# Kernel optimization log

Measured on AMD Instinct MI355X. Metric: run time of the kernel, lower is better.

## Reference

```python
import jax, jax.numpy as jnp
import numpy as np
from jax import lax

N_HEADS = 8
HEAD_DIM = 64
STATE = N_HEADS * HEAD_DIM  # 512
EPS = 1e-6


def setup_inputs() -> dict:
    key = jax.random.key(0)
    ks = jax.random.split(key, 6)
    B, S, D = 4, 4096, 1024
    x = jax.random.normal(ks[0], (B, S, D), jnp.float32)
    w_in = jax.random.normal(ks[1], (4 * STATE, D), jnp.float32) * 0.02
    conv_w = jax.random.normal(ks[2], (STATE, 1, 4), jnp.float32) * 0.5
    state_weight = jax.random.normal(ks[3], (3 * N_HEADS, HEAD_DIM, HEAD_DIM), jnp.float32) * 0.02
    norm_w = jnp.ones((STATE,), jnp.float32)
    w_out = jax.random.normal(ks[5], (D, STATE), jnp.float32) * 0.02
    return {"x": x, "w_in": w_in, "conv_w": conv_w, "state_weight": state_weight, "norm_w": norm_w, "w_out": w_out}


def _forward(x, w_in, conv_w, state_weight, norm_w, w_out):
    B, S, _ = x.shape
    proj = jnp.einsum('bsd,od->bso', x, w_in)  # [B,S,4*STATE]
    xi, xf, xr, g = jnp.split(proj, [STATE, 2 * STATE, 3 * STATE], axis=-1)

    # causal depthwise conv1d on xi (pad left k-1, groups = STATE), then silu
    K = conv_w.shape[-1]
    xi_c = xi.transpose(0, 2, 1)  # [B,C,S]
    xi_c = lax.conv_general_dilated(xi_c, conv_w, window_strides=(1,),
                                    padding=[(K - 1, 0)], feature_group_count=STATE)
    xi = jax.nn.silu(xi_c.transpose(0, 2, 1))  # [B,S,STATE]

    xi = xi.reshape(B, S, N_HEADS, HEAD_DIM)
    xf = xf.reshape(B, S, N_HEADS, HEAD_DIM)
    xr = xr.reshape(B, S, N_HEADS, HEAD_DIM)

    W = state_weight[:N_HEADS]
    Wf = state_weight[N_HEADS:2 * N_HEADS]
    Wr = state_weight[2 * N_HEADS:]

    def step(h, inp):
        xt, xft, xrt = inp  # each [B,N,H]
        f = jax.nn.sigmoid(jnp.einsum('bnh,nhk->bnk', h, Wf) + xft)
        r = jax.nn.sigmoid(jnp.einsum('bnh,nhk->bnk', h, Wr) + xrt)
        z = jnp.tanh(jnp.einsum('bnh,nhk->bnk', h * r, W) + xt)
        h_new = f * h + (1.0 - f) * z
        return h_new, h_new

    h0 = jnp.zeros((B, N_HEADS, HEAD_DIM), x.dtype)
    xs = (xi.transpose(1, 0, 2, 3), xf.transpose(1, 0, 2, 3), xr.transpose(1, 0, 2, 3))
    _, ys = lax.scan(step, h0, xs)  # [S,B,N,H]

    y = ys.transpose(1, 0, 2, 3).reshape(B, S, STATE)
    y = y * jax.nn.silu(g)
    # RMSNorm
    y = y * lax.rsqrt(jnp.mean(y * y, axis=-1, keepdims=True) + EPS) * norm_w
    return jnp.einsum('bss_,os_->bso'.replace('s_', 'c'), y, w_out)


def reference(x, w_in, conv_w, state_weight, norm_w, w_out):
    return _forward(x, w_in, conv_w, state_weight, norm_w, w_out)
```

## Files before the change

### kernel.cpp

```cpp
#include <hip/hip_runtime.h>
#include <hip/hip_bf16.h>
#include <cstddef>

#define B_      4
#define S_      4096
#define D_      1024
#define NH_     8
#define HD_     64
#define STATE_  512
#define PROJ_   2048
#define ROWS_   16384

typedef float f32x4 __attribute__((ext_vector_type(4)));
typedef __bf16 bf16x8 __attribute__((ext_vector_type(8)));
typedef _Float16 f16x2 __attribute__((ext_vector_type(2)));

__device__ __forceinline__ unsigned short bfbits(float f) {
    __hip_bfloat16 h = __float2bfloat16(f);
    return __builtin_bit_cast(unsigned short, h);
}

__device__ __forceinline__ float b2f(unsigned short u) {
    union { unsigned int i; float f; } v;
    v.i = ((unsigned int)u) << 16;
    return v.f;
}

__device__ __forceinline__ float fast_sigmoid(float x) {
    return __builtin_amdgcn_rcpf(1.0f + __expf(-x));
}

__device__ __forceinline__ float fast_tanh(float x) {
    return 1.0f - 2.0f * __builtin_amdgcn_rcpf(__expf(2.0f * x) + 1.0f);
}

__device__ __forceinline__ void async_copy16(void* lds, const void* g) {
    __builtin_amdgcn_global_load_lds(
        (const __attribute__((address_space(1))) unsigned int*)g,
        (__attribute__((address_space(3))) unsigned int*)lds,
        16, 0, 0);
}

__device__ __forceinline__ unsigned int pkf16(float a, float b) {
    auto h = __builtin_amdgcn_cvt_pkrtz(a, b);
    return __builtin_bit_cast(unsigned int, h);
}

__device__ __forceinline__ f16x2 u2h(unsigned int u) {
    return __builtin_bit_cast(f16x2, u);
}

__device__ __forceinline__ unsigned int rl_u32(unsigned int v, int lane) {
    return (unsigned int)__builtin_amdgcn_readlane((int)v, lane);
}

__device__ __forceinline__ float fdot2f(f16x2 a, f16x2 b, float c) {
    return __builtin_amdgcn_fdot2(a, b, c, false);
}

__device__ __forceinline__ unsigned int pack_pair(float v, bool oddlane) {
    int vb = __builtin_bit_cast(int, v);
    int pb = __builtin_amdgcn_mov_dpp(vb, 0xB1, 0xF, 0xF, true);
    float p = __builtin_bit_cast(float, pb);
    float lo = oddlane ? p : v;
    float hi = oddlane ? v : p;
    return pkf16(lo, hi);
}

__global__ __launch_bounds__(256) void f2bf(const float* __restrict__ in,
                                            unsigned short* __restrict__ out, int n4) {
    int i = blockIdx.x * 256 + threadIdx.x;
    if (i < n4) {
        float4 v = ((const float4*)in)[i];
        ushort4 o;
        o.x = bfbits(v.x); o.y = bfbits(v.y); o.z = bfbits(v.z); o.w = bfbits(v.w);
        ((ushort4*)out)[i] = o;
    }
}

__device__ __forceinline__ void store_out(float* p, float v) { *p = v; }
__device__ __forceinline__ void store_out(__hip_bfloat16* p, float v) { *p = __float2bfloat16(v); }

template <typename OutT>
__global__ __launch_bounds__(256, 1) void gemm_bt(const unsigned short* __restrict__ A,
                                                  const unsigned short* __restrict__ Bm,
                                                  OutT* __restrict__ C,
                                                  int M, int N, int K) {
    __shared__ __align__(16) unsigned short As[128 * 32];
    __shared__ __align__(16) unsigned short Bs[128 * 32];
    const int tid  = threadIdx.x;
    const int lane = tid & 63;
    const int w    = tid >> 6;
    const int wm   = w >> 1;
    const int wn   = w & 1;
    const int l16  = lane & 15;
    const int quad = lane >> 4;
    const int m0 = blockIdx.y * 128;
    const int n0 = blockIdx.x * 128;

    f32x4 acc[4][4] = {};

    const int off0 = w * 1024 + lane * 16;
    const int off1 = (w + 4) * 1024 + lane * 16;
    const int r0 = off0 >> 6, cb0 = off0 & 63;
    const int r1 = off1 >> 6, cb1 = off1 & 63;
    char* lA0 = (char*)As + w * 1024;
    char* lA1 = (char*)As + (w + 4) * 1024;
    char* lB0 = (char*)Bs + w * 1024;
    char* lB1 = (char*)Bs + (w + 4) * 1024;
    const size_t Kb = (size_t)K * 2;

    for (int k0 = 0; k0 < K; k0 += 32) {
        const char* a0 = (const char*)A + (size_t)(m0 + r0) * Kb + (size_t)k0 * 2 + cb0;
        const char* a1 = (const char*)A + (size_t)(m0 + r1) * Kb + (size_t)k0 * 2 + cb1;
        const char* b0 = (const char*)Bm + (size_t)(n0 + r0) * Kb + (size_t)k0 * 2 + cb0;
        const char* b1 = (const char*)Bm + (size_t)(n0 + r1) * Kb + (size_t)k0 * 2 + cb1;
        async_copy16(lA0, a0);
        async_copy16(lA1, a1);
        async_copy16(lB0, b0);
        async_copy16(lB1, b1);
        __syncthreads();

        bf16x8 af[4], bf[4];
#pragma unroll
        for (int mt = 0; mt < 4; ++mt) {
            int r = wm * 64 + mt * 16 + l16;
            af[mt] = *(const bf16x8*)(&As[r * 32 + quad * 8]);
        }
#pragma unroll
        for (int nt = 0; nt < 4; ++nt) {
            int r = wn * 64 + nt * 16 + l16;
            bf[nt] = *(const bf16x8*)(&Bs[r * 32 + quad * 8]);
        }
#pragma unroll
        for (int mt = 0; mt < 4; ++mt)
#pragma unroll
            for (int nt = 0; nt < 4; ++nt)
                acc[mt][nt] = __builtin_amdgcn_mfma_f32_16x16x32_bf16(af[mt], bf[nt], acc[mt][nt], 0, 0, 0);
        __syncthreads();
    }

#pragma unroll
    for (int mt = 0; mt < 4; ++mt) {
#pragma unroll
        for (int nt = 0; nt < 4; ++nt) {
            const int col = n0 + wn * 64 + nt * 16 + l16;
            const int row = m0 + wm * 64 + mt * 16 + quad * 4;
#pragma unroll
            for (int rg = 0; rg < 4; ++rg)
                store_out(&C[(size_t)(row + rg) * N + col], acc[mt][nt][rg]);
        }
    }
}

__global__ __launch_bounds__(256) void transpose_scan(const unsigned short* __restrict__ proj,
                                                      ushort4* __restrict__ sc) {
    const int idx = blockIdx.x * 256 + threadIdx.x;
    const int c   = idx & 511;
    const int row = idx >> 9;
    const int b = row >> 12, t = row & 4095;
    const int n = c >> 6, kk = c & 63;
    const unsigned short* src = proj + (size_t)row * PROJ_ + c;
    ushort4 v;
    v.x = src[0];
    v.y = src[512];
    v.z = src[1024];
    v.w = src[1536];
    sc[((size_t)(b * 8 + n) * S_ + t) * 64 + kk] = v;
}

#define SCAN_STEP(T, V)                                                        \
    {                                                                          \
        const float xi_raw = b2f(V.x);                                         \
        const float xf_v   = b2f(V.y);                                         \
        const float xr_v   = b2f(V.z);                                         \
        const float g_v    = b2f(V.w);                                         \
        {                       \
            const int tn = ((T) + 2 < S_) ? (T) + 2 : S_ - 1;                  \
            V = pin[(size_t)tn * 64];                                          \
        }                                                                      \
        float xc = fmaf(cw3, xi_raw, fmaf(cw2, xm1, fmaf(cw1, xm2, cw0 * xm3)));\
        xm3 = xm2; xm2 = xm1; xm1 = xi_raw;                                    \
        const float xi_v = xc * fast_sigmoid(xc);                              \
        const float gs_v = g_v * fast_sigmoid(g_v);                            \
        unsigned int hs[32];                                                   \
        _Pragma("unroll")                                                      \
        for (int p = 0; p < 32; ++p) hs[p] = rl_u32(hpk, 2 * p);               \
        __builtin_amdgcn_sched_barrier(0);                                     \
        float fa[4] = {xf_v, 0.f, 0.f, 0.f};                                   \
        float ra[4] = {xr_v, 0.f, 0.f, 0.f};                                   \
        _Pragma("unroll")                                                      \
        for (int p = 0; p < 32; ++p) {                                         \
            fa[p & 3] = fdot2f(u2h(hs[p]), u2h(Wf2[p]), fa[p & 3]);            \
            ra[p & 3] = fdot2f(u2h(hs[p]), u2h(Wr2[p]), ra[p & 3]);            \
        }                                                                      \
        const float f_v = fast_sigmoid((fa[0] + fa[1]) + (fa[2] + fa[3]));     \
        const float r_v = fast_sigmoid((ra[0] + ra[1]) + (ra[2] + ra[3]));     \
        const unsigned int hrpk = pack_pair(h_me * r_v, oddlane);              \
        __builtin_amdgcn_sched_barrier(0);                                     \
        unsigned int zs[32];                                                   \
        _Pragma("unroll")                                                      \
        for (int p = 0; p < 32; ++p) zs[p] = rl_u32(hrpk, 2 * p);              \
        __builtin_amdgcn_sched_barrier(0);                                     \
        float za[4] = {xi_v, 0.f, 0.f, 0.f};                                   \
        _Pragma("unroll")                                                      \
        for (int p = 0; p < 32; ++p)                                           \
            za[p & 3] = fdot2f(u2h(zs[p]), u2h(Wz2[p]), za[p & 3]);            \
        const float z_v = fast_tanh((za[0] + za[1]) + (za[2] + za[3]));        \
        const float hn  = fmaf(f_v, h_me - z_v, z_v);                          \
        h_me = hn;                                                             \
        hpk  = pack_pair(hn, oddlane);                                         \
        yout[(size_t)(T) * STATE_] = hn * gs_v;                                \
    }

__global__ __launch_bounds__(64)
__attribute__((amdgpu_waves_per_eu(1, 1)))
void scan_kernel(
    const ushort4* __restrict__ scanin,
    const float* __restrict__ conv_w,
    const float* __restrict__ sw,
    float* __restrict__ y)
{
    const int bn = blockIdx.x;
    const int b  = bn >> 3;
    const int n  = bn & 7;
    const int k  = threadIdx.x;
    const int c  = n * HD_ + k;
    const bool oddlane = (k & 1) != 0;

    unsigned int Wz2[32], Wf2[32], Wr2[32];
    {
        const float* wz = sw + (size_t)n * 4096 + k;
        const float* wf = wz + 8 * 4096;
        const float* wr = wz + 16 * 4096;
#pragma unroll
        for (int jp = 0; jp < 32; ++jp) {
            Wz2[jp] = pkf16(wz[(2 * jp) * 64], wz[(2 * jp + 1) * 64]);
            Wf2[jp] = pkf16(wf[(2 * jp) * 64], wf[(2 * jp + 1) * 64]);
            Wr2[jp] = pkf16(wr[(2 * jp) * 64], wr[(2 * jp + 1) * 64]);
        }
    }
    const float cw0 = conv_w[c * 4 + 0];
    const float cw1 = conv_w[c * 4 + 1];
    const float cw2 = conv_w[c * 4 + 2];
    const float cw3 = conv_w[c * 4 + 3];

    float h_me = 0.0f;
    unsigned int hpk = 0;
    float xm1 = 0.f, xm2 = 0.f, xm3 = 0.f;

    const ushort4* pin = scanin + (size_t)bn * S_ * 64 + k;
    float* yout = y + (size_t)b * S_ * STATE_ + c;

    ushort4 aV = pin[0];
    ushort4 bV = pin[64];

    for (int t = 0; t < S_; t += 2) {
        SCAN_STEP(t,     aV);
        SCAN_STEP(t + 1, bV);
    }
}

__global__ __launch_bounds__(128) void rmsnorm_bf16(const float* __restrict__ y,
                                                    const float* __restrict__ nw,
                                                    unsigned short* __restrict__ out) {
    const int row = blockIdx.x;
    const int t   = threadIdx.x;
    const float4 v = ((const float4*)(y + (size_t)row * STATE_))[t];
    float ss = fmaf(v.x, v.x, fmaf(v.y, v.y, fmaf(v.z, v.z, v.w * v.w)));
#pragma unroll
    for (int off = 32; off > 0; off >>= 1) ss += __shfl_xor(ss, off, 64);
    __shared__ float wred[2];
    if ((t & 63) == 0) wred[t >> 6] = ss;
    __syncthreads();
    const float tot   = wred[0] + wred[1];
    const float scale = rsqrtf(tot * (1.0f / (float)STATE_) + 1e-6f);
    const float4 w4 = ((const float4*)nw)[t];
    ushort4 o;
    o.x = bfbits(v.x * scale * w4.x);
    o.y = bfbits(v.y * scale * w4.y);
    o.z = bfbits(v.z * scale * w4.z);
    o.w = bfbits(v.w * scale * w4.w);
    ((ushort4*)out)[(size_t)row * (STATE_ / 4) + t] = o;
}

extern "C" void kernel_launch(void* const* d_in, const int* in_sizes, int n_in,
                              void* d_out, int out_size, void* d_ws, size_t ws_size,
                              hipStream_t stream) {
    const float* x      = (const float*)d_in[0];
    const float* w_in   = (const float*)d_in[1];
    const float* conv_w = (const float*)d_in[2];
    const float* sw     = (const float*)d_in[3];
    const float* norm_w = (const float*)d_in[4];
    const float* w_out  = (const float*)d_in[5];
    float* out = (float*)d_out;

    char* ws = (char*)d_ws;
    unsigned short* xbf     = (unsigned short*)(ws + 0);
    unsigned short* w_inbf  = (unsigned short*)(ws + 33554432);
    unsigned short* w_outbf = (unsigned short*)(ws + 37748736);
    ushort4*        scanin  = (ushort4*)(ws + 38797312);
    float*          yf      = (float*)(ws + 0);
    unsigned short* ybf     = (unsigned short*)(ws + 38797312);
    unsigned short* projbf  = (unsigned short*)d_out;

    f2bf<<<(ROWS_ * D_ / 4 + 255) / 256, 256, 0, stream>>>(x, xbf, ROWS_ * D_ / 4);
    f2bf<<<(PROJ_ * D_ / 4 + 255) / 256, 256, 0, stream>>>(w_in, w_inbf, PROJ_ * D_ / 4);
    f2bf<<<(D_ * STATE_ / 4 + 255) / 256, 256, 0, stream>>>(w_out, w_outbf, D_ * STATE_ / 4);

    gemm_bt<__hip_bfloat16><<<dim3(PROJ_ / 128, ROWS_ / 128), 256, 0, stream>>>(
        xbf, w_inbf, (__hip_bfloat16*)projbf, ROWS_, PROJ_, D_);

    transpose_scan<<<ROWS_ * 512 / 256, 256, 0, stream>>>(projbf, scanin);

    scan_kernel<<<32, 64, 0, stream>>>(scanin, conv_w, sw, yf);

    rmsnorm_bf16<<<ROWS_, 128, 0, stream>>>(yf, norm_w, ybf);

    gemm_bt<float><<<dim3(D_ / 128, ROWS_ / 128), 256, 0, stream>>>(
        ybf, w_outbf, out, ROWS_, D_, STATE_);
}
```

Measured before the change: 2.105 ms.

## Interleave four batch recurrences per wavefront in scan kernel for ILP

The scan kernel now runs one wavefront per head that advances all four batch sequences together, instead of one wavefront per (batch, head). The readlane broadcasts and dot products of independent batches are interleaved so that the serial latency of each recurrence step is hidden by work from the other batches. In exchange the grid shrinks from 32 to 8 wavefronts, so less of the GPU is used, and register pressure rises, with a possible risk of spills.

```diff
diff --git a/kernel.cpp b/kernel.cpp
--- a/kernel.cpp
+++ b/kernel.cpp
@@ -169,48 +169,76 @@
     sc[((size_t)(b * 8 + n) * S_ + t) * 64 + kk] = v;
 }
 
-#define SCAN_STEP(T, V)                                                        \
+
+#define SB __builtin_amdgcn_sched_barrier(0);
+
+#define DECODE(b, T, V)                                                        \
+    const float xf_##b = b2f(V.y);                                             \
+    const float xr_##b = b2f(V.z);                                             \
+    const float g_##b  = b2f(V.w);                                             \
+    float xc_##b;                                                              \
     {                                                                          \
         const float xi_raw = b2f(V.x);                                         \
-        const float xf_v   = b2f(V.y);                                         \
-        const float xr_v   = b2f(V.z);                                         \
-        const float g_v    = b2f(V.w);                                         \
-        {                       \
-            const int tn = ((T) + 2 < S_) ? (T) + 2 : S_ - 1;                  \
-            V = pin[(size_t)tn * 64];                                          \
-        }                                                                      \
-        float xc = fmaf(cw3, xi_raw, fmaf(cw2, xm1, fmaf(cw1, xm2, cw0 * xm3)));\
-        xm3 = xm2; xm2 = xm1; xm1 = xi_raw;                                    \
-        const float xi_v = xc * fast_sigmoid(xc);                              \
-        const float gs_v = g_v * fast_sigmoid(g_v);                            \
-        unsigned int hs[32];                                                   \
-        _Pragma("unroll")                                                      \
-        for (int p = 0; p < 32; ++p) hs[p] = rl_u32(hpk, 2 * p);               \
-        __builtin_amdgcn_sched_barrier(0);                                     \
-        float fa[4] = {xf_v, 0.f, 0.f, 0.f};                                   \
-        float ra[4] = {xr_v, 0.f, 0.f, 0.f};                                   \
-        _Pragma("unroll")                                                      \
-        for (int p = 0; p < 32; ++p) {                                         \
-            fa[p & 3] = fdot2f(u2h(hs[p]), u2h(Wf2[p]), fa[p & 3]);            \
-            ra[p & 3] = fdot2f(u2h(hs[p]), u2h(Wr2[p]), ra[p & 3]);            \
-        }                                                                      \
-        const float f_v = fast_sigmoid((fa[0] + fa[1]) + (fa[2] + fa[3]));     \
-        const float r_v = fast_sigmoid((ra[0] + ra[1]) + (ra[2] + ra[3]));     \
-        const unsigned int hrpk = pack_pair(h_me * r_v, oddlane);              \
-        __builtin_amdgcn_sched_barrier(0);                                     \
-        unsigned int zs[32];                                                   \
-        _Pragma("unroll")                                                      \
-        for (int p = 0; p < 32; ++p) zs[p] = rl_u32(hrpk, 2 * p);              \
-        __builtin_amdgcn_sched_barrier(0);                                     \
-        float za[4] = {xi_v, 0.f, 0.f, 0.f};                                   \
-        _Pragma("unroll")                                                      \
-        for (int p = 0; p < 32; ++p)                                           \
-            za[p & 3] = fdot2f(u2h(zs[p]), u2h(Wz2[p]), za[p & 3]);            \
-        const float z_v = fast_tanh((za[0] + za[1]) + (za[2] + za[3]));        \
-        const float hn  = fmaf(f_v, h_me - z_v, z_v);                          \
-        h_me = hn;                                                             \
-        hpk  = pack_pair(hn, oddlane);                                         \
-        yout[(size_t)(T) * STATE_] = hn * gs_v;                                \
+        const int tn = ((T) + 2 < S_) ? (T) + 2 : S_ - 1;                      \
+        V = pin_##b[(size_t)tn * 64];                                          \
+        xc_##b = fmaf(cw3, xi_raw,                                             \
+                 fmaf(cw2, xm1_##b, fmaf(cw1, xm2_##b, cw0 * xm3_##b)));       \
+        xm3_##b = xm2_##b; xm2_##b = xm1_##b; xm1_##b = xi_raw;                \
+    }                                                                          \
+    const float xiv_##b = xc_##b * fast_sigmoid(xc_##b);                       \
+    const float gsv_##b = g_##b * fast_sigmoid(g_##b);
+
+#define RLB(arr, src)                                                          \
+    _Pragma("unroll")                                                          \
+    for (int p = 0; p < 32; ++p) arr[p] = rl_u32(src, 2 * p);
+
+#define FRD(b, arr)                                                            \
+    float fa_##b[4] = {xf_##b, 0.f, 0.f, 0.f};                                 \
+    float ra_##b[4] = {xr_##b, 0.f, 0.f, 0.f};                                 \
+    _Pragma("unroll")                                                          \
+    for (int p = 0; p < 32; ++p) {                                             \
+        fa_##b[p & 3] = fdot2f(u2h(arr[p]), u2h(Wf2[p]), fa_##b[p & 3]);       \
+        ra_##b[p & 3] = fdot2f(u2h(arr[p]), u2h(Wr2[p]), ra_##b[p & 3]);       \
+    }
+
+#define GAT(b)                                                                 \
+    const float fv_##b = fast_sigmoid((fa_##b[0] + fa_##b[1]) +                \
+                                      (fa_##b[2] + fa_##b[3]));                \
+    const float rv_##b = fast_sigmoid((ra_##b[0] + ra_##b[1]) +                \
+                                      (ra_##b[2] + ra_##b[3]));                \
+    const unsigned int hr_##b = pack_pair(h_##b * rv_##b, oddlane);
+
+#define ZD(b, arr)                                                             \
+    float za_##b[4] = {xiv_##b, 0.f, 0.f, 0.f};                                \
+    _Pragma("unroll")                                                          \
+    for (int p = 0; p < 32; ++p)                                               \
+        za_##b[p & 3] = fdot2f(u2h(arr[p]), u2h(Wz2[p]), za_##b[p & 3]);
+
+#define UPD(b, T)                                                              \
+    {                                                                          \
+        const float zv = fast_tanh((za_##b[0] + za_##b[1]) +                   \
+                                   (za_##b[2] + za_##b[3]));                   \
+        const float hn = fmaf(fv_##b, h_##b - zv, zv);                         \
+        h_##b  = hn;                                                           \
+        hp_##b = pack_pair(hn, oddlane);                                       \
+        yout_##b[(size_t)(T) * STATE_] = hn * gsv_##b;                         \
+    }
+
+#define STEP4(T, V0, V1, V2, V3)                                               \
+    {                                                                          \
+        DECODE(0, T, V0) DECODE(1, T, V1) DECODE(2, T, V2) DECODE(3, T, V3)    \
+        unsigned int hsA[32], hsB[32];                                         \
+        RLB(hsA, hp_0) RLB(hsB, hp_1) SB                                       \
+        FRD(0, hsA) FRD(1, hsB) SB                                             \
+        RLB(hsA, hp_2) RLB(hsB, hp_3) SB                                       \
+        GAT(0) GAT(1)                                                          \
+        FRD(2, hsA) FRD(3, hsB) SB                                             \
+        GAT(2) GAT(3)                                                          \
+        RLB(hsA, hr_0) RLB(hsB, hr_1) SB                                       \
+        ZD(0, hsA) ZD(1, hsB) SB                                               \
+        RLB(hsA, hr_2) RLB(hsB, hr_3) SB                                       \
+        ZD(2, hsA) ZD(3, hsB)                                                  \
+        UPD(0, T) UPD(1, T) UPD(2, T) UPD(3, T)                                \
     }
 
 __global__ __launch_bounds__(64)
@@ -221,11 +249,9 @@
     const float* __restrict__ sw,
     float* __restrict__ y)
 {
-    const int bn = blockIdx.x;
-    const int b  = bn >> 3;
-    const int n  = bn & 7;
-    const int k  = threadIdx.x;
-    const int c  = n * HD_ + k;
+    const int n = blockIdx.x;
+    const int k = threadIdx.x;
+    const int c = n * HD_ + k;
     const bool oddlane = (k & 1) != 0;
 
     unsigned int Wz2[32], Wf2[32], Wr2[32];
@@ -245,19 +271,30 @@
     const float cw2 = conv_w[c * 4 + 2];
     const float cw3 = conv_w[c * 4 + 3];
 
-    float h_me = 0.0f;
-    unsigned int hpk = 0;
-    float xm1 = 0.f, xm2 = 0.f, xm3 = 0.f;
-
-    const ushort4* pin = scanin + (size_t)bn * S_ * 64 + k;
-    float* yout = y + (size_t)b * S_ * STATE_ + c;
-
-    ushort4 aV = pin[0];
-    ushort4 bV = pin[64];
+    float h_0 = 0.f, h_1 = 0.f, h_2 = 0.f, h_3 = 0.f;
+    unsigned int hp_0 = 0, hp_1 = 0, hp_2 = 0, hp_3 = 0;
+    float xm1_0 = 0.f, xm2_0 = 0.f, xm3_0 = 0.f;
+    float xm1_1 = 0.f, xm2_1 = 0.f, xm3_1 = 0.f;
+    float xm1_2 = 0.f, xm2_2 = 0.f, xm3_2 = 0.f;
+    float xm1_3 = 0.f, xm2_3 = 0.f, xm3_3 = 0.f;
+
+    const ushort4* pin_0 = scanin + (size_t)(0 * 8 + n) * S_ * 64 + k;
+    const ushort4* pin_1 = scanin + (size_t)(1 * 8 + n) * S_ * 64 + k;
+    const ushort4* pin_2 = scanin + (size_t)(2 * 8 + n) * S_ * 64 + k;
+    const ushort4* pin_3 = scanin + (size_t)(3 * 8 + n) * S_ * 64 + k;
+    float* yout_0 = y + (size_t)0 * S_ * STATE_ + c;
+    float* yout_1 = y + (size_t)1 * S_ * STATE_ + c;
+    float* yout_2 = y + (size_t)2 * S_ * STATE_ + c;
+    float* yout_3 = y + (size_t)3 * S_ * STATE_ + c;
+
+    ushort4 pA0 = pin_0[0], pB0 = pin_0[64];
+    ushort4 pA1 = pin_1[0], pB1 = pin_1[64];
+    ushort4 pA2 = pin_2[0], pB2 = pin_2[64];
+    ushort4 pA3 = pin_3[0], pB3 = pin_3[64];
 
     for (int t = 0; t < S_; t += 2) {
-        SCAN_STEP(t,     aV);
-        SCAN_STEP(t + 1, bV);
+        STEP4(t,     pA0, pA1, pA2, pA3);
+        STEP4(t + 1, pB0, pB1, pB2, pB3);
     }
 }
 
@@ -313,7 +350,7 @@
 
     transpose_scan<<<ROWS_ * 512 / 256, 256, 0, stream>>>(projbf, scanin);
 
-    scan_kernel<<<32, 64, 0, stream>>>(scanin, conv_w, sw, yf);
+    scan_kernel<<<8, 64, 0, stream>>>(scanin, conv_w, sw, yf);
 
     rmsnorm_bf16<<<ROWS_, 128, 0, stream>>>(yf, norm_w, ybf);
 
```

After: 7.166 ms. 240% more time.
